# Performance work log

Measured on AMD Instinct MI355X. Metric: run time of the kernel, lower is better.

Reference implementation:

```python
import jax, jax.numpy as jnp
import numpy as np
from jax import lax

EPS = 1e-7  # keras.backend.epsilon()
DT = 0.05

def _k(a):
    # (3,3) -> HWIO (3,3,1,1) fp32 kernel constant
    return jnp.asarray(np.asarray(a, dtype=np.float32).reshape(3, 3, 1, 1))

KXP = _k([[0,0,0],[0,-1,1],[0,0,0]])
KXN = _k([[0,0,0],[-1,1,0],[0,0,0]])
KYP = _k([[0,1,0],[0,-1,0],[0,0,0]])
KYN = _k([[0,0,0],[0,1,0],[0,-1,0]])
KXC = _k([[0,0,0],[-1,0,1],[0,0,0]])
KYC = _k([[0,1,0],[0,0,0],[0,-1,0]])
KLX = _k([[1,0,-1],[2,0,-2],[1,0,-1]])
KLY = _k([[1,2,1],[0,0,0],[-1,-2,-1]])

def conv(x, k):
    # TF K.conv2d 'same' == XLA cross-correlation, NHWC/HWIO
    return lax.conv_general_dilated(x, k, (1, 1), 'SAME',
                                    dimension_numbers=('NHWC', 'HWIO', 'NHWC'))

def setup_inputs() -> dict:
    key = jax.random.key(0)
    k1, k2 = jax.random.split(key)
    B, H, W = 32, 512, 512
    u = jax.random.normal(k1, (B, H, W, 1), dtype=jnp.float32)
    img = jax.random.uniform(k2, (B, H, W, 1), dtype=jnp.float32)
    alpha = jnp.ones((1, 1, 1, 1), jnp.float32)
    beta = jnp.ones((1, 1, 1, 1), jnp.float32)
    gamma = jnp.ones((1, 1, 1, 1), jnp.float32)
    return {"u": u, "img": img, "alpha": alpha, "beta": beta, "gamma": gamma}

def reference(u, img, alpha, beta, gamma):
    # --- edge stopping function g(img) (precomputed in build() in original) ---
    ex = conv(img, KLX)
    ey = conv(img, KLY)
    edges = jnp.square(jnp.square(ex) + jnp.square(ey))
    edges = edges / jnp.max(edges)
    edges = 1.0 / (edges + 1.0)
    gex = conv(edges, KXC)
    gey = conv(edges, KYC)
    # --- upwind transport term ---
    xp = conv(u, KXP); xn = conv(u, KXN)
    yp = conv(u, KYP); yn = conv(u, KYN)
    fxp = jax.nn.relu(gex); fxn = -jax.nn.relu(-gex)
    fyp = jax.nn.relu(gey); fyn = -jax.nn.relu(-gey)
    transport = 20.0 * ((fxp * xp + fxn * xn) + (fyp * yp + fyn * yn))
    # --- curvature (divergence of normalized gradient) ---
    gux = conv(u, KXC)
    guy = conv(u, KYC)
    normu = jnp.sqrt(jnp.square(gux) + jnp.square(guy) + EPS)
    kappa = conv(gux / (normu + EPS), KXC) + conv(guy / (normu + EPS), KYC)
    curvature = edges * kappa * normu
    balloon = edges * normu
    return u + DT * (curvature * alpha + transport * beta + balloon * gamma)
```

## Files before the change

### kernel.cpp

```cpp
#include <hip/hip_runtime.h>

#define HH 512
#define WW 512
#define NB 32
#define EPSF 1e-7f
#define DTF 0.05f
#define RS1 2
#define RSF 2

__device__ __forceinline__ float bperm(int addr, float v) {
    return __int_as_float(__builtin_amdgcn_ds_bpermute(addr, __float_as_int(v)));
}

struct R10 { float v[10]; };

template<bool EDGE>
__device__ __forceinline__ void load_row10(const float* __restrict__ base, int row,
                                           int c4, int jl, int jr,
                                           bool lo, bool hi, R10& r) {
    int rc = row;
    if (EDGE) rc = min(max(row, 0), HH - 1);
    const float* __restrict__ rp = base + rc * WW;
    const float4* p = (const float4*)(rp + c4);
    float4 a = p[0], b = p[1];
    float l = rp[jl], h = rp[jr];
    if (EDGE && ((unsigned)row >= (unsigned)HH)) {
        a.x = a.y = a.z = a.w = 0.f;
        b.x = b.y = b.z = b.w = 0.f;
        l = 0.f; h = 0.f;
    }
    r.v[0] = lo ? 0.f : l;
    r.v[1] = a.x; r.v[2] = a.y; r.v[3] = a.z; r.v[4] = a.w;
    r.v[5] = b.x; r.v[6] = b.y; r.v[7] = b.z; r.v[8] = b.w;
    r.v[9] = hi ? 0.f : h;
}

template<bool EDGE>
__device__ __forceinline__ float e4_strip(const float* __restrict__ IM, int i0,
                                          int c4, int jl, int jr, bool lo, bool hi) {
    R10 A, B, C;
    load_row10<EDGE>(IM, i0 - 1, c4, jl, jr, lo, hi, A);
    load_row10<EDGE>(IM, i0,     c4, jl, jr, lo, hi, B);
    float m = 0.f;
    #pragma unroll
    for (int i = i0; i < i0 + RS1; ++i) {
        load_row10<EDGE>(IM, i + 1, c4, jl, jr, lo, hi, C);
        #pragma unroll
        for (int k = 1; k <= 8; ++k) {
            float ex = (A.v[k-1] - A.v[k+1]) + 2.f * (B.v[k-1] - B.v[k+1]) + (C.v[k-1] - C.v[k+1]);
            float ey = (A.v[k-1] - C.v[k-1]) + 2.f * (A.v[k] - C.v[k]) + (A.v[k+1] - C.v[k+1]);
            float s2 = ex * ex + ey * ey;
            m = fmaxf(m, s2 * s2);
        }
        A = B; B = C;
    }
    return m;
}

__global__ __launch_bounds__(256)
void max_e4_kernel(const float* __restrict__ img, float* __restrict__ partial) {
    const int wid  = blockIdx.x * 4 + (threadIdx.x >> 6);
    const int lane = threadIdx.x & 63;
    const int rs = wid & 255;
    const int b  = wid >> 8;
    const int i0 = rs * RS1;
    const float* __restrict__ IM = img + (size_t)b * (HH * WW);
    const bool lo = (lane == 0), hi = (lane == 63);
    const int c4 = 8 * lane;
    const int jl = max(c4 - 1, 0), jr = min(c4 + 8, WW - 1);

    float m = (rs == 0 || rs == 255)
        ? e4_strip<true >(IM, i0, c4, jl, jr, lo, hi)
        : e4_strip<false>(IM, i0, c4, jl, jr, lo, hi);

    for (int off = 32; off > 0; off >>= 1)
        m = fmaxf(m, __shfl_down(m, off, 64));
    if (lane == 0) partial[wid] = m;
}

__global__ __launch_bounds__(256)
void reduce_max(const float* __restrict__ partial, float* __restrict__ wsmax) {
    const float4* p4 = (const float4*)partial;
    float v = 0.f;
    #pragma unroll
    for (int k = 0; k < 8; ++k) {
        float4 a = p4[threadIdx.x + 256 * k];
        v = fmaxf(v, fmaxf(fmaxf(a.x, a.y), fmaxf(a.z, a.w)));
    }
    for (int off = 32; off > 0; off >>= 1)
        v = fmaxf(v, __shfl_down(v, off, 64));
    __shared__ float smax[4];
    const int lane = threadIdx.x & 63, w = threadIdx.x >> 6;
    if (lane == 0) smax[w] = v;
    __syncthreads();
    if (threadIdx.x == 0)
        wsmax[0] = fmaxf(fmaxf(smax[0], smax[1]), fmaxf(smax[2], smax[3]));
}

template<bool EDGE>
__device__ __forceinline__ void ff_impl(const float* __restrict__ U,
                                        const float* __restrict__ IM,
                                        float* __restrict__ O,
                                        int o0, int c4, int jl, int jr,
                                        int bpu, int bpd,
                                        bool lo, bool hi, float M,
                                        float dta, float dtb, float dtg) {
    R10 I0, I1, R1, R2, E2 = {}, PX2 = {};
    float R0[9] = {}, E1[9] = {}, PY1[9] = {}, PY2[9] = {};

    load_row10<EDGE>(IM, o0 - 2, c4, jl, jr, lo, hi, I0);
    load_row10<EDGE>(IM, o0 - 1, c4, jl, jr, lo, hi, I1);
    load_row10<EDGE>(U,  o0 - 2, c4, jl, jr, lo, hi, R1);
    load_row10<EDGE>(U,  o0 - 1, c4, jl, jr, lo, hi, R2);

    #pragma unroll
    for (int o = o0 - 2; o < o0 + RSF; ++o) {
        R10 C, W;
        load_row10<EDGE>(IM, o + 2, c4, jl, jr, lo, hi, C);
        load_row10<EDGE>(U,  o + 2, c4, jl, jr, lo, hi, W);

        R10 eN, PXN;
        float PYN[9];
        const bool zrow = EDGE && (o < -1 || o >= HH - 1);
        #pragma unroll
        for (int k = 1; k <= 8; ++k) {
            float ex = (I0.v[k-1] - I0.v[k+1]) + 2.f * (I1.v[k-1] - I1.v[k+1]) + (C.v[k-1] - C.v[k+1]);
            float ey = (I0.v[k-1] - C.v[k-1]) + 2.f * (I0.v[k] - C.v[k]) + (I0.v[k+1] - C.v[k+1]);
            float s2 = ex * ex + ey * ey;
            float e  = M * __builtin_amdgcn_rcpf(s2 * s2 + M);
            float gux = R2.v[k+1] - R2.v[k-1];
            float guy = R1.v[k] - W.v[k];
            float rn  = __builtin_amdgcn_rsqf(gux * gux + guy * guy + EPSF);
            eN.v[k]  = zrow ? 0.f : e;
            PXN.v[k] = zrow ? 0.f : gux * rn;
            PYN[k]   = zrow ? 0.f : guy * rn;
        }
        {
            float a = bperm(bpu, eN.v[8]),  bb = bperm(bpd, eN.v[1]);
            float c = bperm(bpu, PXN.v[8]), d  = bperm(bpd, PXN.v[1]);
            eN.v[0]  = lo ? 0.f : a;  eN.v[9]  = hi ? 0.f : bb;
            PXN.v[0] = lo ? 0.f : c;  PXN.v[9] = hi ? 0.f : d;
        }

        if (o >= o0) {
            float vals[8];
            #pragma unroll
            for (int k = 1; k <= 8; ++k) {
                float gex = E2.v[k+1] - E2.v[k-1];
                float gey = E1[k] - eN.v[k];
                float xp = R1.v[k+1] - R1.v[k], xn = R1.v[k] - R1.v[k-1];
                float yp = R0[k] - R1.v[k],     yn = R1.v[k] - R2.v[k];
                float tr = fmaxf(gex, 0.f) * xp + fminf(gex, 0.f) * xn
                         + fmaxf(gey, 0.f) * yp + fminf(gey, 0.f) * yn;
                float gxc = R1.v[k+1] - R1.v[k-1], gyc = R0[k] - R2.v[k];
                float ncv = __builtin_amdgcn_sqrtf(gxc * gxc + gyc * gyc + EPSF);
                float kap = (PX2.v[k+1] - PX2.v[k-1]) + (PY1[k] - PYN[k]);
                vals[k-1] = R1.v[k] + E2.v[k] * ncv * (kap * dta + dtg) + tr * dtb;
            }
            float4* p = (float4*)(O + o * WW + c4);
            p[0] = make_float4(vals[0], vals[1], vals[2], vals[3]);
            p[1] = make_float4(vals[4], vals[5], vals[6], vals[7]);
        }

        I0 = I1; I1 = C;
        #pragma unroll
        for (int k = 1; k <= 8; ++k) { R0[k] = R1.v[k]; E1[k] = E2.v[k]; PY1[k] = PY2[k]; PY2[k] = PYN[k]; }
        R1 = R2; R2 = W;
        E2 = eN; PX2 = PXN;
    }
}

__global__ __launch_bounds__(256)
void fused_ff(const float* __restrict__ u, const float* __restrict__ img,
              const float* __restrict__ pa, const float* __restrict__ pb,
              const float* __restrict__ pg, const float* __restrict__ wsmax,
              float* __restrict__ out) {
    const int wid  = blockIdx.x * 4 + (threadIdx.x >> 6);
    const int lane = threadIdx.x & 63;
    const int rs = wid & 255;
    const int b  = wid >> 8;
    const int o0 = rs * RSF;
    const size_t base = (size_t)b * (HH * WW);
    const bool lo = (lane == 0), hi = (lane == 63);
    const int c4 = 8 * lane;
    const int jl = max(c4 - 1, 0), jr = min(c4 + 8, WW - 1);
    const int bpu = ((lane + 63) & 63) << 2, bpd = ((lane + 1) & 63) << 2;

    const float M   = wsmax[0];
    const float dta = DTF * pa[0];
    const float dtb = 20.f * DTF * pb[0];
    const float dtg = DTF * pg[0];

    if (rs == 0 || rs == 255)
        ff_impl<true >(u + base, img + base, out + base, o0, c4, jl, jr, bpu, bpd, lo, hi, M, dta, dtb, dtg);
    else
        ff_impl<false>(u + base, img + base, out + base, o0, c4, jl, jr, bpu, bpd, lo, hi, M, dta, dtb, dtg);
}

extern "C" void kernel_launch(void* const* d_in, const int* in_sizes, int n_in,
                              void* d_out, int out_size, void* d_ws, size_t ws_size,
                              hipStream_t stream) {
    const float* u   = (const float*)d_in[0];
    const float* img = (const float*)d_in[1];
    const float* pa  = (const float*)d_in[2];
    const float* pb  = (const float*)d_in[3];
    const float* pg  = (const float*)d_in[4];
    float* out = (float*)d_out;
    float* partial = (float*)d_ws;
    float* wsmax   = partial + 8192;

    max_e4_kernel<<<2048, 256, 0, stream>>>(img, partial);
    reduce_max<<<1, 256, 0, stream>>>(partial, wsmax);
    fused_ff<<<2048, 256, 0, stream>>>(u, img, pa, pb, pg, wsmax, out);
}
```

Baseline: 138.2 us.

## Replace scalar halo loads with lane permutes and batch row loads up front

Row loads now fetch only the 8 owned floats per lane, and the left and right halo values come from neighbouring lanes through ds_bpermute instead of extra scalar global loads. The max kernel's strip height is doubled, halving its grid and the partial-reduction size. Both kernels issue all row loads before computing, replacing the rolling-window loop, to expose more memory-level parallelism. This costs more registers and more permute traffic.

```diff
diff --git a/kernel.cpp b/kernel.cpp
--- a/kernel.cpp
+++ b/kernel.cpp
@@ -5,7 +5,7 @@
 #define NB 32
 #define EPSF 1e-7f
 #define DTF 0.05f
-#define RS1 2
+#define RS1 4
 #define RSF 2
 
 __device__ __forceinline__ float bperm(int addr, float v) {
@@ -13,46 +13,56 @@
 }
 
 struct R10 { float v[10]; };
+struct F8  { float v[8]; };
 
 template<bool EDGE>
-__device__ __forceinline__ void load_row10(const float* __restrict__ base, int row,
-                                           int c4, int jl, int jr,
-                                           bool lo, bool hi, R10& r) {
+__device__ __forceinline__ void load_row8(const float* __restrict__ base, int row,
+                                          int c4, F8& r) {
     int rc = row;
     if (EDGE) rc = min(max(row, 0), HH - 1);
-    const float* __restrict__ rp = base + rc * WW;
-    const float4* p = (const float4*)(rp + c4);
+    const float4* p = (const float4*)(base + rc * WW + c4);
     float4 a = p[0], b = p[1];
-    float l = rp[jl], h = rp[jr];
     if (EDGE && ((unsigned)row >= (unsigned)HH)) {
         a.x = a.y = a.z = a.w = 0.f;
         b.x = b.y = b.z = b.w = 0.f;
-        l = 0.f; h = 0.f;
-    }
+    }
+    r.v[0] = a.x; r.v[1] = a.y; r.v[2] = a.z; r.v[3] = a.w;
+    r.v[4] = b.x; r.v[5] = b.y; r.v[6] = b.z; r.v[7] = b.w;
+}
+
+__device__ __forceinline__ void expand(const F8& s, int bpu, int bpd,
+                                       bool lo, bool hi, R10& r) {
+    #pragma unroll
+    for (int k = 0; k < 8; ++k) r.v[k + 1] = s.v[k];
+    float l = bperm(bpu, s.v[7]);
+    float h = bperm(bpd, s.v[0]);
     r.v[0] = lo ? 0.f : l;
-    r.v[1] = a.x; r.v[2] = a.y; r.v[3] = a.z; r.v[4] = a.w;
-    r.v[5] = b.x; r.v[6] = b.y; r.v[7] = b.z; r.v[8] = b.w;
     r.v[9] = hi ? 0.f : h;
 }
 
 template<bool EDGE>
 __device__ __forceinline__ float e4_strip(const float* __restrict__ IM, int i0,
-                                          int c4, int jl, int jr, bool lo, bool hi) {
-    R10 A, B, C;
-    load_row10<EDGE>(IM, i0 - 1, c4, jl, jr, lo, hi, A);
-    load_row10<EDGE>(IM, i0,     c4, jl, jr, lo, hi, B);
+                                          int c4, int bpu, int bpd, bool lo, bool hi) {
+    F8 raw[RS1 + 2];
+    #pragma unroll
+    for (int s = 0; s < RS1 + 2; ++s)
+        load_row8<EDGE>(IM, i0 - 1 + s, c4, raw[s]);
+    R10 I[RS1 + 2];
+    #pragma unroll
+    for (int s = 0; s < RS1 + 2; ++s)
+        expand(raw[s], bpu, bpd, lo, hi, I[s]);
     float m = 0.f;
     #pragma unroll
-    for (int i = i0; i < i0 + RS1; ++i) {
-        load_row10<EDGE>(IM, i + 1, c4, jl, jr, lo, hi, C);
+    for (int t = 0; t < RS1; ++t) {
         #pragma unroll
         for (int k = 1; k <= 8; ++k) {
-            float ex = (A.v[k-1] - A.v[k+1]) + 2.f * (B.v[k-1] - B.v[k+1]) + (C.v[k-1] - C.v[k+1]);
-            float ey = (A.v[k-1] - C.v[k-1]) + 2.f * (A.v[k] - C.v[k]) + (A.v[k+1] - C.v[k+1]);
+            float ex = (I[t].v[k-1] - I[t].v[k+1]) + 2.f * (I[t+1].v[k-1] - I[t+1].v[k+1])
+                     + (I[t+2].v[k-1] - I[t+2].v[k+1]);
+            float ey = (I[t].v[k-1] - I[t+2].v[k-1]) + 2.f * (I[t].v[k] - I[t+2].v[k])
+                     + (I[t].v[k+1] - I[t+2].v[k+1]);
             float s2 = ex * ex + ey * ey;
             m = fmaxf(m, s2 * s2);
         }
-        A = B; B = C;
     }
     return m;
 }
@@ -61,17 +71,17 @@
 void max_e4_kernel(const float* __restrict__ img, float* __restrict__ partial) {
     const int wid  = blockIdx.x * 4 + (threadIdx.x >> 6);
     const int lane = threadIdx.x & 63;
-    const int rs = wid & 255;
-    const int b  = wid >> 8;
+    const int rs = wid & 127;
+    const int b  = wid >> 7;
     const int i0 = rs * RS1;
     const float* __restrict__ IM = img + (size_t)b * (HH * WW);
     const bool lo = (lane == 0), hi = (lane == 63);
     const int c4 = 8 * lane;
-    const int jl = max(c4 - 1, 0), jr = min(c4 + 8, WW - 1);
-
-    float m = (rs == 0 || rs == 255)
-        ? e4_strip<true >(IM, i0, c4, jl, jr, lo, hi)
-        : e4_strip<false>(IM, i0, c4, jl, jr, lo, hi);
+    const int bpu = ((lane + 63) & 63) << 2, bpd = ((lane + 1) & 63) << 2;
+
+    float m = (rs == 0 || rs == 127)
+        ? e4_strip<true >(IM, i0, c4, bpu, bpd, lo, hi)
+        : e4_strip<false>(IM, i0, c4, bpu, bpd, lo, hi);
 
     for (int off = 32; off > 0; off >>= 1)
         m = fmaxf(m, __shfl_down(m, off, 64));
@@ -83,7 +93,7 @@
     const float4* p4 = (const float4*)partial;
     float v = 0.f;
     #pragma unroll
-    for (int k = 0; k < 8; ++k) {
+    for (int k = 0; k < 4; ++k) {
         float4 a = p4[threadIdx.x + 256 * k];
         v = fmaxf(v, fmaxf(fmaxf(a.x, a.y), fmaxf(a.z, a.w)));
     }
@@ -101,72 +111,72 @@
 __device__ __forceinline__ void ff_impl(const float* __restrict__ U,
                                         const float* __restrict__ IM,
                                         float* __restrict__ O,
-                                        int o0, int c4, int jl, int jr,
-                                        int bpu, int bpd,
+                                        int o0, int c4, int bpu, int bpd,
                                         bool lo, bool hi, float M,
                                         float dta, float dtb, float dtg) {
-    R10 I0, I1, R1, R2, E2 = {}, PX2 = {};
-    float R0[9] = {}, E1[9] = {}, PY1[9] = {}, PY2[9] = {};
-
-    load_row10<EDGE>(IM, o0 - 2, c4, jl, jr, lo, hi, I0);
-    load_row10<EDGE>(IM, o0 - 1, c4, jl, jr, lo, hi, I1);
-    load_row10<EDGE>(U,  o0 - 2, c4, jl, jr, lo, hi, R1);
-    load_row10<EDGE>(U,  o0 - 1, c4, jl, jr, lo, hi, R2);
-
-    #pragma unroll
-    for (int o = o0 - 2; o < o0 + RSF; ++o) {
-        R10 C, W;
-        load_row10<EDGE>(IM, o + 2, c4, jl, jr, lo, hi, C);
-        load_row10<EDGE>(U,  o + 2, c4, jl, jr, lo, hi, W);
-
-        R10 eN, PXN;
-        float PYN[9];
-        const bool zrow = EDGE && (o < -1 || o >= HH - 1);
+    F8 imr[6], uur[6];
+    #pragma unroll
+    for (int s = 0; s < 6; ++s) load_row8<EDGE>(IM, o0 - 2 + s, c4, imr[s]);
+    #pragma unroll
+    for (int s = 0; s < 6; ++s) load_row8<EDGE>(U,  o0 - 2 + s, c4, uur[s]);
+
+    R10 I[6], Uu[6];
+    #pragma unroll
+    for (int s = 0; s < 6; ++s) expand(imr[s], bpu, bpd, lo, hi, I[s]);
+    #pragma unroll
+    for (int s = 0; s < 6; ++s) expand(uur[s], bpu, bpd, lo, hi, Uu[s]);
+
+    R10 E[4], PX[2];
+    float PY[4][8];
+    #pragma unroll
+    for (int rr = 0; rr < 4; ++rr) {
+        const bool zrow = EDGE && ((unsigned)(o0 - 1 + rr) >= (unsigned)HH);
         #pragma unroll
         for (int k = 1; k <= 8; ++k) {
-            float ex = (I0.v[k-1] - I0.v[k+1]) + 2.f * (I1.v[k-1] - I1.v[k+1]) + (C.v[k-1] - C.v[k+1]);
-            float ey = (I0.v[k-1] - C.v[k-1]) + 2.f * (I0.v[k] - C.v[k]) + (I0.v[k+1] - C.v[k+1]);
+            float ex = (I[rr].v[k-1] - I[rr].v[k+1]) + 2.f * (I[rr+1].v[k-1] - I[rr+1].v[k+1])
+                     + (I[rr+2].v[k-1] - I[rr+2].v[k+1]);
+            float ey = (I[rr].v[k-1] - I[rr+2].v[k-1]) + 2.f * (I[rr].v[k] - I[rr+2].v[k])
+                     + (I[rr].v[k+1] - I[rr+2].v[k+1]);
             float s2 = ex * ex + ey * ey;
             float e  = M * __builtin_amdgcn_rcpf(s2 * s2 + M);
-            float gux = R2.v[k+1] - R2.v[k-1];
-            float guy = R1.v[k] - W.v[k];
+            float gux = Uu[rr+1].v[k+1] - Uu[rr+1].v[k-1];
+            float guy = Uu[rr].v[k] - Uu[rr+2].v[k];
             float rn  = __builtin_amdgcn_rsqf(gux * gux + guy * guy + EPSF);
-            eN.v[k]  = zrow ? 0.f : e;
-            PXN.v[k] = zrow ? 0.f : gux * rn;
-            PYN[k]   = zrow ? 0.f : guy * rn;
+            E[rr].v[k]  = zrow ? 0.f : e;
+            PY[rr][k-1] = zrow ? 0.f : guy * rn;
+            if (rr == 1 || rr == 2)
+                PX[rr-1].v[k] = zrow ? 0.f : gux * rn;
         }
-        {
-            float a = bperm(bpu, eN.v[8]),  bb = bperm(bpd, eN.v[1]);
-            float c = bperm(bpu, PXN.v[8]), d  = bperm(bpd, PXN.v[1]);
-            eN.v[0]  = lo ? 0.f : a;  eN.v[9]  = hi ? 0.f : bb;
-            PXN.v[0] = lo ? 0.f : c;  PXN.v[9] = hi ? 0.f : d;
+    }
+    #pragma unroll
+    for (int rr = 1; rr <= 2; ++rr) {
+        float a = bperm(bpu, E[rr].v[8]),      bb = bperm(bpd, E[rr].v[1]);
+        float c = bperm(bpu, PX[rr-1].v[8]),   d  = bperm(bpd, PX[rr-1].v[1]);
+        E[rr].v[0]    = lo ? 0.f : a;  E[rr].v[9]    = hi ? 0.f : bb;
+        PX[rr-1].v[0] = lo ? 0.f : c;  PX[rr-1].v[9] = hi ? 0.f : d;
+    }
+
+    #pragma unroll
+    for (int oo = 0; oo < 2; ++oo) {
+        float vals[8];
+        #pragma unroll
+        for (int k = 1; k <= 8; ++k) {
+            float gex = E[oo+1].v[k+1] - E[oo+1].v[k-1];
+            float gey = E[oo].v[k] - E[oo+2].v[k];
+            float uc = Uu[oo+2].v[k];
+            float xp = Uu[oo+2].v[k+1] - uc, xn = uc - Uu[oo+2].v[k-1];
+            float yp = Uu[oo+1].v[k] - uc,   yn = uc - Uu[oo+3].v[k];
+            float tr = fmaxf(gex, 0.f) * xp + fminf(gex, 0.f) * xn
+                     + fmaxf(gey, 0.f) * yp + fminf(gey, 0.f) * yn;
+            float gxc = Uu[oo+2].v[k+1] - Uu[oo+2].v[k-1];
+            float gyc = Uu[oo+1].v[k] - Uu[oo+3].v[k];
+            float ncv = __builtin_amdgcn_sqrtf(gxc * gxc + gyc * gyc + EPSF);
+            float kap = (PX[oo].v[k+1] - PX[oo].v[k-1]) + (PY[oo][k-1] - PY[oo+2][k-1]);
+            vals[k-1] = uc + E[oo+1].v[k] * ncv * (kap * dta + dtg) + tr * dtb;
         }
-
-        if (o >= o0) {
-            float vals[8];
-            #pragma unroll
-            for (int k = 1; k <= 8; ++k) {
-                float gex = E2.v[k+1] - E2.v[k-1];
-                float gey = E1[k] - eN.v[k];
-                float xp = R1.v[k+1] - R1.v[k], xn = R1.v[k] - R1.v[k-1];
-                float yp = R0[k] - R1.v[k],     yn = R1.v[k] - R2.v[k];
-                float tr = fmaxf(gex, 0.f) * xp + fminf(gex, 0.f) * xn
-                         + fmaxf(gey, 0.f) * yp + fminf(gey, 0.f) * yn;
-                float gxc = R1.v[k+1] - R1.v[k-1], gyc = R0[k] - R2.v[k];
-                float ncv = __builtin_amdgcn_sqrtf(gxc * gxc + gyc * gyc + EPSF);
-                float kap = (PX2.v[k+1] - PX2.v[k-1]) + (PY1[k] - PYN[k]);
-                vals[k-1] = R1.v[k] + E2.v[k] * ncv * (kap * dta + dtg) + tr * dtb;
-            }
-            float4* p = (float4*)(O + o * WW + c4);
-            p[0] = make_float4(vals[0], vals[1], vals[2], vals[3]);
-            p[1] = make_float4(vals[4], vals[5], vals[6], vals[7]);
-        }
-
-        I0 = I1; I1 = C;
-        #pragma unroll
-        for (int k = 1; k <= 8; ++k) { R0[k] = R1.v[k]; E1[k] = E2.v[k]; PY1[k] = PY2[k]; PY2[k] = PYN[k]; }
-        R1 = R2; R2 = W;
-        E2 = eN; PX2 = PXN;
+        float4* p = (float4*)(O + (o0 + oo) * WW + c4);
+        p[0] = make_float4(vals[0], vals[1], vals[2], vals[3]);
+        p[1] = make_float4(vals[4], vals[5], vals[6], vals[7]);
     }
 }
 
@@ -183,7 +193,6 @@
     const size_t base = (size_t)b * (HH * WW);
     const bool lo = (lane == 0), hi = (lane == 63);
     const int c4 = 8 * lane;
-    const int jl = max(c4 - 1, 0), jr = min(c4 + 8, WW - 1);
     const int bpu = ((lane + 63) & 63) << 2, bpd = ((lane + 1) & 63) << 2;
 
     const float M   = wsmax[0];
@@ -192,9 +201,9 @@
     const float dtg = DTF * pg[0];
 
     if (rs == 0 || rs == 255)
-        ff_impl<true >(u + base, img + base, out + base, o0, c4, jl, jr, bpu, bpd, lo, hi, M, dta, dtb, dtg);
+        ff_impl<true >(u + base, img + base, out + base, o0, c4, bpu, bpd, lo, hi, M, dta, dtb, dtg);
     else
-        ff_impl<false>(u + base, img + base, out + base, o0, c4, jl, jr, bpu, bpd, lo, hi, M, dta, dtb, dtg);
+        ff_impl<false>(u + base, img + base, out + base, o0, c4, bpu, bpd, lo, hi, M, dta, dtb, dtg);
 }
 
 extern "C" void kernel_launch(void* const* d_in, const int* in_sizes, int n_in,
@@ -207,9 +216,9 @@
     const float* pg  = (const float*)d_in[4];
     float* out = (float*)d_out;
     float* partial = (float*)d_ws;
-    float* wsmax   = partial + 8192;
-
-    max_e4_kernel<<<2048, 256, 0, stream>>>(img, partial);
+    float* wsmax   = partial + 4096;
+
+    max_e4_kernel<<<1024, 256, 0, stream>>>(img, partial);
     reduce_max<<<1, 256, 0, stream>>>(partial, wsmax);
     fused_ff<<<2048, 256, 0, stream>>>(u, img, pa, pb, pg, wsmax, out);
 }
```

Measured after the change: 128.9 us. 1.07x faster.
